# Optimization experiments

Hardware: AMD Instinct MI355X
Metric: run time of the kernel (lower is better)

The kernel has to match this reference:

```python
import jax, jax.numpy as jnp
import numpy as np

N, E, G = 8192, 65536, 16          # atoms, edges, graphs in batch
NUM_ELEM, C, NB = 10, 64, 8        # elements, hidden channels, bessel basis
LMAX, NLAYERS = 3, 2
LM = (LMAX + 1) ** 2               # 16 spherical-harmonic components
R_MAX, P_CUT = 5.0, 5
EPS = 1e-9


def spherical_harmonics(u):
    # u: [E,3] unit vectors -> real spherical harmonics l<=3, [E,16]
    x, y, z = u[:, 0], u[:, 1], u[:, 2]
    x2, y2, z2 = x * x, y * y, z * z
    sh = [
        jnp.full_like(x, 0.28209479177387814),
        0.4886025119029199 * y, 0.4886025119029199 * z, 0.4886025119029199 * x,
        1.0925484305920792 * x * y, 1.0925484305920792 * y * z,
        0.31539156525252005 * (3.0 * z2 - 1.0),
        1.0925484305920792 * x * z, 0.5462742152960396 * (x2 - y2),
        0.5900435899266435 * y * (3.0 * x2 - y2), 2.890611442640554 * x * y * z,
        0.4570457994644658 * y * (5.0 * z2 - 1.0),
        0.3731763325901154 * z * (5.0 * z2 - 3.0),
        0.4570457994644658 * x * (5.0 * z2 - 1.0),
        1.445305721320277 * z * (x2 - y2),
        0.5900435899266435 * x * (x2 - 3.0 * y2),
    ]
    return jnp.stack(sh, axis=-1)


def radial_embedding(r):
    # Bessel radial basis with polynomial envelope cutoff -> [E, NB]
    u = r / R_MAX
    p = float(P_CUT)
    cut = (1.0 - 0.5 * (p + 1.0) * (p + 2.0) * u ** P_CUT
           + p * (p + 2.0) * u ** (P_CUT + 1)
           - 0.5 * p * (p + 1.0) * u ** (P_CUT + 2))
    cut = jnp.where(u < 1.0, cut, 0.0)
    n = jnp.arange(1, NB + 1, dtype=r.dtype)
    bessel = jnp.sqrt(2.0 / R_MAX) * jnp.sin(n[None, :] * jnp.pi * u[:, None]) \
             / jnp.maximum(r, EPS)[:, None]
    return bessel * cut[:, None]


def setup_inputs() -> dict:
    key = jax.random.key(0)
    ks = jax.random.split(key, 10)
    positions = jax.random.uniform(ks[0], (N, 3), jnp.float32) * 10.0
    elems = jax.random.randint(ks[1], (N,), 0, NUM_ELEM)
    node_attrs = jax.nn.one_hot(elems, NUM_ELEM, dtype=jnp.float32)
    edge_index = jax.random.randint(ks[2], (2, E), 0, N).astype(jnp.int32)
    shifts = jnp.zeros((E, 3), jnp.float32)
    batch = jnp.sort(jax.random.randint(ks[3], (N,), 0, G)).astype(jnp.int32)
    W_embed = jax.random.normal(ks[4], (NUM_ELEM, C), jnp.float32) / np.sqrt(NUM_ELEM)
    atomic_energies_w = jnp.arange(-1.0, -(NUM_ELEM + 1.0), -1.0, dtype=jnp.float32)
    W_rad = jax.random.normal(ks[5], (NLAYERS, NB, C), jnp.float32) / np.sqrt(NB)
    W_prod = jax.random.normal(ks[6], (NLAYERS, NUM_ELEM, (LMAX + 1) * C, C),
                               jnp.float32) / np.sqrt((LMAX + 1) * C)
    w_read = jax.random.normal(ks[7], (C,), jnp.float32) / np.sqrt(C)
    return {"positions": positions, "node_attrs": node_attrs, "shifts": shifts,
            "W_embed": W_embed, "atomic_energies_w": atomic_energies_w,
            "W_rad": W_rad, "W_prod": W_prod, "w_read": w_read,
            "edge_index": edge_index, "batch": batch}


def _energy(positions, node_attrs, shifts, W_embed, atomic_energies_w,
            W_rad, W_prod, w_read, edge_index, batch):
    snd, rcv = edge_index[0], edge_index[1]
    vec = positions[rcv] - positions[snd] + shifts            # [E,3]
    length = jnp.sqrt(jnp.sum(vec * vec, axis=-1) + EPS)      # [E]
    Y = spherical_harmonics(vec / length[:, None])            # [E,LM]
    R = radial_embedding(length)                              # [E,NB]

    e0 = jax.ops.segment_sum(node_attrs @ atomic_energies_w, batch, num_segments=G)
    h = node_attrs @ W_embed                                  # [N,C]

    for layer in range(NLAYERS):
        w = R @ W_rad[layer]                                  # [E,C] radial weights
        msg = (w * h[snd])[:, None, :] * Y[:, :, None]        # [E,LM,C] tensor product
        A = jax.ops.segment_sum(msg, rcv, num_segments=N)     # [N,LM,C] atomic basis
        A2 = A * A
        # invariant (rotation-invariant) contraction: sum over m within each l
        B = jnp.concatenate(
            [A2[:, l * l:(l + 1) * (l + 1), :].sum(axis=1) for l in range(LMAX + 1)],
            axis=-1)                                          # [N,(LMAX+1)*C]
        # element-dependent product-basis mixing
        h = jnp.einsum('nf,efc,ne->nc', B, W_prod[layer], node_attrs)

    node_e = h @ w_read                                       # [N]
    inter_e = jax.ops.segment_sum(node_e, batch, num_segments=G)
    return e0 + inter_e                                       # [G]


def reference(positions, node_attrs, shifts, W_embed, atomic_energies_w,
              W_rad, W_prod, w_read, edge_index, batch):
    energy = _energy(positions, node_attrs, shifts, W_embed, atomic_energies_w,
                     W_rad, W_prod, w_read, edge_index, batch)
    forces = -jax.grad(
        lambda p: _energy(p, node_attrs, shifts, W_embed, atomic_energies_w,
                          W_rad, W_prod, w_read, edge_index, batch).sum()
    )(positions)
    return energy, forces
```

## Files before the change

### kernel.cpp

```cpp
#include <hip/hip_runtime.h>
#include <math.h>

#define NN 8192
#define NE 65536
#define NG 16
#define NEL 10
#define CC 64
#define NLM 16
#define MAXST 32
#define PI_F 3.14159265358979f

__device__ __forceinline__ int lm_l(int lm) {
    return (lm == 0) ? 0 : (lm < 4) ? 1 : (lm < 9) ? 2 : 3;
}

__device__ __forceinline__ void stage_pack(
    const float* __restrict__ PK, const int* __restrict__ SSND,
    int beg, int cnt, int c, float* sPK, int* sS)
{
    int tot = cnt * 24;
    for (int i = c; i < tot; i += 64) sPK[i] = PK[(size_t)beg*24 + i];
    if (c < cnt) sS[c] = SSND[beg + c];
    __builtin_amdgcn_wave_barrier();
}

__global__ __launch_bounds__(256) void k_front(
    const float* __restrict__ pos, const float* __restrict__ shifts,
    const int* __restrict__ snd, const int* __restrict__ rcv,
    float* __restrict__ Y, float* __restrict__ R,
    float* __restrict__ U, float* __restrict__ L, int* __restrict__ cnt,
    const float* __restrict__ attrs, const float* __restrict__ Wemb,
    const float* __restrict__ aew, const int* __restrict__ batch,
    float* __restrict__ h0, int* __restrict__ elem, int* __restrict__ ecnt,
    float* __restrict__ out,
    const float* __restrict__ Wprod1, const float* __restrict__ wread,
    float* __restrict__ vb1)
{
    __shared__ int hcnt[NEL];
    int bx = blockIdx.x;
    if (bx < 256) {
        int e = bx * 256 + threadIdx.x;
        int s = snd[e], r = rcv[e];
        float vx = pos[r*3+0] - pos[s*3+0] + shifts[e*3+0];
        float vy = pos[r*3+1] - pos[s*3+1] + shifts[e*3+1];
        float vz = pos[r*3+2] - pos[s*3+2] + shifts[e*3+2];
        float len = sqrtf(vx*vx + vy*vy + vz*vz + 1e-9f);
        L[e] = len;
        if (len >= 5.0f) return;
        atomicAdd(&cnt[r], 1);
        float x = vx/len, y = vy/len, z = vz/len;
        U[e*3+0] = x; U[e*3+1] = y; U[e*3+2] = z;
        float x2 = x*x, y2 = y*y, z2 = z*z;
        float4* Yv = (float4*)(Y + (size_t)e*16);
        Yv[0] = make_float4(0.28209479177387814f,
                            0.4886025119029199f*y,
                            0.4886025119029199f*z,
                            0.4886025119029199f*x);
        Yv[1] = make_float4(1.0925484305920792f*x*y,
                            1.0925484305920792f*y*z,
                            0.31539156525252005f*(3.f*z2 - 1.f),
                            1.0925484305920792f*x*z);
        Yv[2] = make_float4(0.5462742152960396f*(x2 - y2),
                            0.5900435899266435f*y*(3.f*x2 - y2),
                            2.890611442640554f*x*y*z,
                            0.4570457994644658f*y*(5.f*z2 - 1.f));
        Yv[3] = make_float4(0.3731763325901154f*z*(5.f*z2 - 3.f),
                            0.4570457994644658f*x*(5.f*z2 - 1.f),
                            1.445305721320277f*z*(x2 - y2),
                            0.5900435899266435f*x*(x2 - 3.f*y2));
        float ur = len * 0.2f;
        float u2 = ur*ur, u4 = u2*u2, u5 = u4*ur, u6 = u5*ur, u7 = u6*ur;
        float cut = 1.f - 21.f*u5 + 35.f*u6 - 15.f*u7;
        const float s2f = 0.632455532033676f;
        float th = (PI_F/5.f) * len;
        float s1, c1; sincosf(th, &s1, &c1);
        float sn_ = s1, cs = c1;
        float coef = s2f * cut / len;
        float rv[8];
#pragma unroll
        for (int nb = 0; nb < 8; nb++) {
            rv[nb] = coef * sn_;
            float ns = sn_*c1 + cs*s1;
            float nc = cs*c1 - sn_*s1;
            sn_ = ns; cs = nc;
        }
        float4* Rv = (float4*)(R + (size_t)e*8);
        Rv[0] = make_float4(rv[0], rv[1], rv[2], rv[3]);
        Rv[1] = make_float4(rv[4], rv[5], rv[6], rv[7]);
    } else if (bx < 768) {
        int t = threadIdx.x, c = t & 63, w = t >> 6;
        if (t < NEL) hcnt[t] = 0;
        __syncthreads();
        float esum = 0.f; int curb = -1;
        for (int g = 0; g < 4; g++) {
            int n = (bx - 256)*16 + w*4 + g;
            float hv = 0.f;
            for (int el = 0; el < NEL; el++) hv += attrs[n*NEL+el] * Wemb[el*CC+c];
            h0[(size_t)n*CC+c] = hv;
            int el = 0; float e0 = 0.f;
            for (int k = 0; k < NEL; k++) {
                float a = attrs[n*NEL+k];
                e0 += a * aew[k];
                if (a > 0.5f) el = k;
            }
            if (c == 0) {
                elem[n] = el;
                atomicAdd(&hcnt[el], 1);
            }
            int b = batch[n];
            if (b != curb) {
                if (curb >= 0 && c == 0) atomicAdd(&out[curb], esum);
                curb = b; esum = 0.f;
            }
            esum += e0;
        }
        if (curb >= 0 && c == 0) atomicAdd(&out[curb], esum);
        __syncthreads();
        if (t < NEL) { int v = hcnt[t]; if (v) atomicAdd(&ecnt[t], v); }
    } else {
        int el = bx - 768, f = threadIdx.x;
        float s = 0.f;
        for (int c = 0; c < CC; c++) s += wread[c] * Wprod1[(size_t)el*256*CC + f*CC + c];
        vb1[el*256+f] = s;
    }
}

__global__ __launch_bounds__(1024) void k_scan(
    const int* __restrict__ cnt, int* __restrict__ offs,
    const int* __restrict__ ecnt, int* __restrict__ eoff)
{
    __shared__ int wsum[16];
    int t = threadIdx.x, lane = t & 63, w = t >> 6;
    int loc[8];
    int run = 0;
#pragma unroll
    for (int i = 0; i < 8; i++) { int v = cnt[t*8+i]; loc[i] = run; run += v; }
    int v = run;
#pragma unroll
    for (int o = 1; o < 64; o <<= 1) {
        int u = __shfl_up(v, o, 64);
        if (lane >= o) v += u;
    }
    if (lane == 63) wsum[w] = v;
    __syncthreads();
    if (t < 16) {
        int x = wsum[t];
#pragma unroll
        for (int o = 1; o < 16; o <<= 1) {
            int u = __shfl_up(x, o, 64);
            if (t >= o) x += u;
        }
        wsum[t] = x;
    }
    __syncthreads();
    int wpre = (w == 0) ? 0 : wsum[w-1];
    int pre = wpre + v - run;
#pragma unroll
    for (int i = 0; i < 8; i++) offs[t*8+i] = pre + loc[i];
    if (t == 1023) offs[NN] = pre + run;
    if (t == 0) {
        int r = 0;
        for (int el = 0; el < NEL; el++) { eoff[el] = r; r += ecnt[el]; }
        eoff[NEL] = r;
    }
}

__global__ void k_scatpack(
    const int* __restrict__ snd, const int* __restrict__ rcv,
    const float* __restrict__ Y, const float* __restrict__ R,
    const float* __restrict__ U, const float* __restrict__ L,
    const int* __restrict__ offs, int* __restrict__ cur,
    float* __restrict__ PK, int* __restrict__ SSND,
    float* __restrict__ UL,
    const int* __restrict__ elem, const int* __restrict__ eoff,
    int* __restrict__ ecur, int* __restrict__ nbe)
{
    int e = blockIdx.x * blockDim.x + threadIdx.x;
    if (e < NN) {
        int el = elem[e];
        int p = eoff[el] + atomicAdd(&ecur[el], 1);
        nbe[p] = e;
    }
    if (e >= NE) return;
    if (L[e] >= 5.0f) return;
    int r = rcv[e];
    int p = offs[r] + atomicAdd(&cur[r], 1);
    const float4* Yp = (const float4*)(Y + (size_t)e*16);
    float4* d = (float4*)(PK + (size_t)p*24);
    d[0] = Yp[0]; d[1] = Yp[1]; d[2] = Yp[2]; d[3] = Yp[3];
    const float4* Rp = (const float4*)(R + (size_t)e*8);
    d[4] = Rp[0]; d[5] = Rp[1];
    SSND[p] = snd[e];
    ((float4*)UL)[p] = make_float4(U[e*3+0], U[e*3+1], U[e*3+2], L[e]);
}

__global__ __launch_bounds__(256) void k_fwd0(
    const float* __restrict__ PK, const int* __restrict__ SSND,
    const float* __restrict__ Wrad0, const float* __restrict__ Wprod0,
    const float* __restrict__ h0, const float* __restrict__ attrs,
    const int* __restrict__ elem, const int* __restrict__ offs,
    const int* __restrict__ nbe, float* __restrict__ h1,
    float* __restrict__ A0)
{
    __shared__ __align__(16) float sB[4][1024];
    __shared__ __align__(16) float sPK[4][MAXST*24];
    __shared__ int sS[4][MAXST];
    int t = threadIdx.x, c = t & 63, w = t >> 6;
    float wr[8];
#pragma unroll
    for (int nb = 0; nb < 8; nb++) wr[nb] = Wrad0[nb*CC+c];
    int nid[4], nel[4]; float na[4];
#pragma unroll
    for (int g = 0; g < 4; g++) {
        int n = nbe[blockIdx.x*16 + w*4 + g];
        nid[g] = n;
        int el = elem[n]; nel[g] = el; na[g] = attrs[n*NEL+el];
        float acc[NLM];
#pragma unroll
        for (int lm = 0; lm < NLM; lm++) acc[lm] = 0.f;
        int beg = offs[n], end = offs[n+1];
        for (int base = beg; base < end; base += MAXST) {
            int m = min(MAXST, end - base);
            stage_pack(PK, SSND, base, m, c, sPK[w], sS[w]);
            for (int cb = 0; cb < m; cb += 4) {
                float hb[4];
#pragma unroll
                for (int k = 0; k < 4; k++)
                    hb[k] = (cb+k < m) ? h0[(size_t)sS[w][cb+k]*CC + c] : 0.f;
#pragma unroll
                for (int jj = 0; jj < 4; jj++) {
                    if (cb+jj >= m) break;
                    const float* rec = &sPK[w][(cb+jj)*24];
                    float wv = 0.f;
#pragma unroll
                    for (int nb = 0; nb < 8; nb++) wv += rec[16+nb]*wr[nb];
                    float tt = wv * hb[jj];
#pragma unroll
                    for (int lm = 0; lm < NLM; lm++) acc[lm] += rec[lm]*tt;
                }
            }
            __builtin_amdgcn_wave_barrier();
        }
#pragma unroll
        for (int lm = 0; lm < NLM; lm++) A0[(size_t)n*1024 + lm*64 + c] = acc[lm];
        float b0 = acc[0]*acc[0];
        float b1 = acc[1]*acc[1] + acc[2]*acc[2] + acc[3]*acc[3];
        float b2 = acc[4]*acc[4] + acc[5]*acc[5] + acc[6]*acc[6] + acc[7]*acc[7] + acc[8]*acc[8];
        float b3 = 0.f;
#pragma unroll
        for (int lm = 9; lm < 16; lm++) b3 += acc[lm]*acc[lm];
        sB[w][g*256 + 0*64 + c] = b0;
        sB[w][g*256 + 1*64 + c] = b1;
        sB[w][g*256 + 2*64 + c] = b2;
        sB[w][g*256 + 3*64 + c] = b3;
    }
    __builtin_amdgcn_wave_barrier();
    float hv[4] = {0.f, 0.f, 0.f, 0.f};
    int done = 0;
    while (done != 0xF) {
        int g0 = __ffs(~done & 0xF) - 1;
        int el = (g0==0) ? nel[0] : (g0==1) ? nel[1] : (g0==2) ? nel[2] : nel[3];
        int msk = 0;
#pragma unroll
        for (int g = 0; g < 4; g++) if (nel[g] == el) msk |= 1 << g;
        const float* Wn = Wprod0 + (size_t)el*256*CC;
        float tmp[4] = {0.f, 0.f, 0.f, 0.f};
        for (int f4 = 0; f4 < 64; f4++) {
            float wv0 = Wn[(f4*4+0)*CC + c];
            float wv1 = Wn[(f4*4+1)*CC + c];
            float wv2 = Wn[(f4*4+2)*CC + c];
            float wv3 = Wn[(f4*4+3)*CC + c];
#pragma unroll
            for (int g = 0; g < 4; g++) {
                float4 b = *((const float4*)&sB[w][g*256 + f4*4]);
                tmp[g] += b.x*wv0 + b.y*wv1 + b.z*wv2 + b.w*wv3;
            }
        }
#pragma unroll
        for (int g = 0; g < 4; g++) if ((msk >> g) & 1) hv[g] = tmp[g];
        done |= msk;
    }
#pragma unroll
    for (int g = 0; g < 4; g++) h1[(size_t)nid[g]*CC + c] = na[g]*hv[g];
}

__global__ __launch_bounds__(256) void k_fbwd1(
    const float* __restrict__ PK, const int* __restrict__ SSND,
    const float* __restrict__ Wrad1, const float* __restrict__ h1,
    const float* __restrict__ vb1,
    const float* __restrict__ attrs, const int* __restrict__ elem,
    const int* __restrict__ batch, const int* __restrict__ offs,
    float* __restrict__ gYp, float* __restrict__ gRp, float* __restrict__ gh,
    float* __restrict__ out)
{
    __shared__ __align__(16) float wrls[8*68];
    __shared__ __align__(16) float sPK[4][MAXST*24];
    __shared__ int sS[4][MAXST];
    __shared__ __align__(16) float Mls[4][16*68];
    __shared__ __align__(16) float Tls[4][4*68];
    __shared__ __align__(16) float Gls[4][4*68];
    int t = threadIdx.x, c = t & 63, w = t >> 6;
    float wr[8];
#pragma unroll
    for (int nb = 0; nb < 8; nb++) wr[nb] = Wrad1[nb*CC+c];
    if (w == 0) {
#pragma unroll
        for (int nb = 0; nb < 8; nb++) wrls[nb*68+c] = wr[nb];
    }
    __syncthreads();
    float esum = 0.f; int curb = -1;
    for (int g = 0; g < 4; g++) {
        int n = blockIdx.x*16 + w*4 + g;
        int el = elem[n];
        float a = attrs[n*NEL+el];
        float g4[4];
#pragma unroll
        for (int l = 0; l < 4; l++) g4[l] = a * vb1[el*256 + l*64 + c];
        int beg = offs[n], end = offs[n+1];
        int cnt = end - beg;
        float acc[NLM];
#pragma unroll
        for (int lm = 0; lm < NLM; lm++) acc[lm] = 0.f;
        for (int base = beg; base < end; base += MAXST) {
            int m = min(MAXST, end - base);
            stage_pack(PK, SSND, base, m, c, sPK[w], sS[w]);
            for (int cb = 0; cb < m; cb += 4) {
                float hb[4];
#pragma unroll
                for (int k = 0; k < 4; k++)
                    hb[k] = (cb+k < m) ? h1[(size_t)sS[w][cb+k]*CC + c] : 0.f;
#pragma unroll
                for (int jj = 0; jj < 4; jj++) {
                    if (cb+jj >= m) break;
                    const float* rec = &sPK[w][(cb+jj)*24];
                    float wv = 0.f;
#pragma unroll
                    for (int nb = 0; nb < 8; nb++) wv += rec[16+nb]*wr[nb];
                    float tt = wv * hb[jj];
#pragma unroll
                    for (int lm = 0; lm < NLM; lm++) acc[lm] += rec[lm]*tt;
                }
            }
            __builtin_amdgcn_wave_barrier();
        }
        bool cached = (cnt <= MAXST);
        float b0 = acc[0]*acc[0];
        float b1 = acc[1]*acc[1] + acc[2]*acc[2] + acc[3]*acc[3];
        float b2 = acc[4]*acc[4] + acc[5]*acc[5] + acc[6]*acc[6] + acc[7]*acc[7] + acc[8]*acc[8];
        float b3 = 0.f;
#pragma unroll
        for (int lm = 9; lm < 16; lm++) b3 += acc[lm]*acc[lm];
        float ep = b0*vb1[el*256+c] + b1*vb1[el*256+64+c]
                 + b2*vb1[el*256+128+c] + b3*vb1[el*256+192+c];
#pragma unroll
        for (int o = 32; o > 0; o >>= 1) ep += __shfl_xor(ep, o, 64);
        int b = batch[n];
        if (b != curb) {
            if (curb >= 0 && c == 0) atomicAdd(&out[curb], esum);
            curb = b; esum = 0.f;
        }
        esum += a * ep;
        float M[NLM];
#pragma unroll
        for (int lm = 0; lm < NLM; lm++) {
            M[lm] = 2.f * acc[lm] * g4[lm_l(lm)];
            Mls[w][lm*68+c] = M[lm];
        }
        __builtin_amdgcn_wave_barrier();
        for (int base = beg; base < end; base += MAXST) {
            int m = min(MAXST, end - base);
            if (!cached) stage_pack(PK, SSND, base, m, c, sPK[w], sS[w]);
            for (int cb = 0; cb < m; cb += 4) {
                int ncq = min(4, m - cb);
                float hb[4];
#pragma unroll
                for (int k = 0; k < 4; k++)
                    hb[k] = (cb+k < m) ? h1[(size_t)sS[w][cb+k]*CC + c] : 0.f;
#pragma unroll
                for (int jj = 0; jj < 4; jj++) {
                    if (jj >= ncq) break;
                    const float* rec = &sPK[w][(cb+jj)*24];
                    float wv = 0.f;
#pragma unroll
                    for (int nb = 0; nb < 8; nb++) wv += rec[16+nb]*wr[nb];
                    float hvv = hb[jj];
                    float my = 0.f;
#pragma unroll
                    for (int lm = 0; lm < NLM; lm++) my += M[lm]*rec[lm];
                    Tls[w][jj*68+c] = wv * hvv;
                    Gls[w][jj*68+c] = hvv * my;
                    atomicAdd(&gh[(size_t)sS[w][cb+jj]*CC + c], wv * my);
                }
                __builtin_amdgcn_wave_barrier();
                {
                    int jj = c >> 4, lm = c & 15;
                    if (jj < ncq) {
                        const float4* mrow = (const float4*)&Mls[w][lm*68];
                        const float4* trow = (const float4*)&Tls[w][jj*68];
                        float s_ = 0.f;
#pragma unroll
                        for (int k4 = 0; k4 < 16; k4++) {
                            float4 mm = mrow[k4]; float4 tv = trow[k4];
                            s_ += mm.x*tv.x + mm.y*tv.y + mm.z*tv.z + mm.w*tv.w;
                        }
                        gYp[(size_t)(base + cb + jj)*16+lm] = s_;
                    }
                }
                if (c < 32) {
                    int jj = c >> 3, nb = c & 7;
                    if (jj < ncq) {
                        const float4* wrow = (const float4*)&wrls[nb*68];
                        const float4* grow = (const float4*)&Gls[w][jj*68];
                        float s_ = 0.f;
#pragma unroll
                        for (int k4 = 0; k4 < 16; k4++) {
                            float4 wv4 = wrow[k4]; float4 gv = grow[k4];
                            s_ += wv4.x*gv.x + wv4.y*gv.y + wv4.z*gv.z + wv4.w*gv.w;
                        }
                        gRp[(size_t)(base + cb + jj)*8+nb] = s_;
                    }
                }
                __builtin_amdgcn_wave_barrier();
            }
        }
    }
    if (curb >= 0 && c == 0) atomicAdd(&out[curb], esum);
}

__global__ __launch_bounds__(256) void k_fbwd0geo(
    const float* __restrict__ PK, const int* __restrict__ SSND,
    const float* __restrict__ Wrad0, const float* __restrict__ h0,
    const float* __restrict__ gh1, const float* __restrict__ Wprod0,
    const float* __restrict__ A0,
    const float* __restrict__ attrs, const int* __restrict__ elem,
    const int* __restrict__ offs, const int* __restrict__ nbe,
    const float* __restrict__ gYp, const float* __restrict__ gRp,
    const float* __restrict__ UL, float* __restrict__ F)
{
    __shared__ __align__(16) float wrls[8*68];
    __shared__ __align__(16) float sPK[4][MAXST*24];
    __shared__ int sS[4][MAXST];
    __shared__ __align__(16) float Mls[4][16*68];
    __shared__ __align__(16) float Tls[4][4*68];
    __shared__ __align__(16) float Gls[4][4*68];
    __shared__ __align__(16) float sgh[4][4][64];
    __shared__ float gols[4][4*24];
    int t = threadIdx.x, c = t & 63, w = t >> 6;
    float wr[8];
#pragma unroll
    for (int nb = 0; nb < 8; nb++) wr[nb] = Wrad0[nb*CC+c];
    if (w == 0) {
#pragma unroll
        for (int nb = 0; nb < 8; nb++) wrls[nb*68+c] = wr[nb];
    }
    __syncthreads();
    int nid[4], nel[4]; float na[4];
#pragma unroll
    for (int g = 0; g < 4; g++) {
        int n = nbe[blockIdx.x*16 + w*4 + g];
        nid[g] = n;
        int el = elem[n]; nel[g] = el; na[g] = attrs[n*NEL+el];
        sgh[w][g][c] = gh1[(size_t)n*CC + c];
    }
    __builtin_amdgcn_wave_barrier();
    float outv[4][4];
    int done = 0;
    while (done != 0xF) {
        int g0 = __ffs(~done & 0xF) - 1;
        int el = (g0==0) ? nel[0] : (g0==1) ? nel[1] : (g0==2) ? nel[2] : nel[3];
        int msk = 0;
#pragma unroll
        for (int g = 0; g < 4; g++) if (nel[g] == el) msk |= 1 << g;
        const float* W0 = Wprod0 + (size_t)el*256*CC;
#pragma unroll
        for (int l = 0; l < 4; l++) {
            const float4* row = (const float4*)(W0 + (size_t)(l*64 + c)*CC);
            float t4[4] = {0.f, 0.f, 0.f, 0.f};
#pragma unroll 4
            for (int k4 = 0; k4 < 16; k4++) {
                float4 wv = row[k4];
#pragma unroll
                for (int g = 0; g < 4; g++) {
                    float4 gg = *((const float4*)&sgh[w][g][k4*4]);
                    t4[g] += wv.x*gg.x + wv.y*gg.y + wv.z*gg.z + wv.w*gg.w;
                }
            }
#pragma unroll
            for (int g = 0; g < 4; g++) if ((msk >> g) & 1) outv[l][g] = t4[g];
        }
        done |= msk;
    }
    for (int g = 0; g < 4; g++) {
        int n = nid[g];
        float g4[4];
#pragma unroll
        for (int l = 0; l < 4; l++) g4[l] = na[g]*outv[l][g];
        int beg = offs[n], end = offs[n+1];
        float acc[NLM];
#pragma unroll
        for (int lm = 0; lm < NLM; lm++) acc[lm] = A0[(size_t)n*1024 + lm*64 + c];
        float M[NLM];
#pragma unroll
        for (int lm = 0; lm < NLM; lm++) {
            M[lm] = 2.f * acc[lm] * g4[lm_l(lm)];
            Mls[w][lm*68+c] = M[lm];
        }
        __builtin_amdgcn_wave_barrier();
        for (int base = beg; base < end; base += MAXST) {
            int m = min(MAXST, end - base);
            stage_pack(PK, SSND, base, m, c, sPK[w], sS[w]);
            for (int cb = 0; cb < m; cb += 4) {
                int ncq = min(4, m - cb);
                float hb[4];
#pragma unroll
                for (int k = 0; k < 4; k++)
                    hb[k] = (cb+k < m) ? h0[(size_t)sS[w][cb+k]*CC + c] : 0.f;
#pragma unroll
                for (int jj = 0; jj < 4; jj++) {
                    if (jj >= ncq) break;
                    const float* rec = &sPK[w][(cb+jj)*24];
                    float wv = 0.f;
#pragma unroll
                    for (int nb = 0; nb < 8; nb++) wv += rec[16+nb]*wr[nb];
                    float hvv = hb[jj];
                    float my = 0.f;
#pragma unroll
                    for (int lm = 0; lm < NLM; lm++) my += M[lm]*rec[lm];
                    Tls[w][jj*68+c] = wv * hvv;
                    Gls[w][jj*68+c] = hvv * my;
                }
                __builtin_amdgcn_wave_barrier();
                {
                    int jj = c >> 4, lm = c & 15;
                    if (jj < ncq) {
                        const float4* mrow = (const float4*)&Mls[w][lm*68];
                        const float4* trow = (const float4*)&Tls[w][jj*68];
                        float s_ = 0.f;
#pragma unroll
                        for (int k4 = 0; k4 < 16; k4++) {
                            float4 mm = mrow[k4]; float4 tv = trow[k4];
                            s_ += mm.x*tv.x + mm.y*tv.y + mm.z*tv.z + mm.w*tv.w;
                        }
                        gols[w][jj*24+lm] = s_ + gYp[(size_t)(base + cb + jj)*16+lm];
                    }
                }
                if (c < 32) {
                    int jj = c >> 3, nb = c & 7;
                    if (jj < ncq) {
                        const float4* wrow = (const float4*)&wrls[nb*68];
                        const float4* grow = (const float4*)&Gls[w][jj*68];
                        float s_ = 0.f;
#pragma unroll
                        for (int k4 = 0; k4 < 16; k4++) {
                            float4 wv4 = wrow[k4]; float4 gv = grow[k4];
                            s_ += wv4.x*gv.x + wv4.y*gv.y + wv4.z*gv.z + wv4.w*gv.w;
                        }
                        gols[w][jj*24+16+nb] = s_ + gRp[(size_t)(base + cb + jj)*8+nb];
                    }
                }
                __builtin_amdgcn_wave_barrier();
                if ((c & 15) == 0) {
                    int jj = c >> 4;
                    if (jj < ncq) {
                        int p = base + cb + jj;
                        const float* go = &gols[w][jj*24];
                        float4 ul = ((const float4*)UL)[p];
                        float x = ul.x, y = ul.y, z = ul.z, len = ul.w;
                        float x2 = x*x, y2 = y*y, z2 = z*z;
                        float gx = 0.f, gy = 0.f, gz = 0.f;
                        gx += 0.4886025119029199f*go[3];
                        gy += 0.4886025119029199f*go[1];
                        gz += 0.4886025119029199f*go[2];
                        gx += 1.0925484305920792f*y*go[4];  gy += 1.0925484305920792f*x*go[4];
                        gy += 1.0925484305920792f*z*go[5];  gz += 1.0925484305920792f*y*go[5];
                        gz += 1.8923493915151203f*z*go[6];
                        gx += 1.0925484305920792f*z*go[7];  gz += 1.0925484305920792f*x*go[7];
                        gx += 1.0925484305920792f*x*go[8];  gy -= 1.0925484305920792f*y*go[8];
                        gx += 3.540261539559861f*x*y*go[9];
                        gy += 0.5900435899266435f*(3.f*x2 - 3.f*y2)*go[9];
                        gx += 2.890611442640554f*y*z*go[10]; gy += 2.890611442640554f*x*z*go[10]; gz += 2.890611442640554f*x*y*go[10];
                        gy += 0.4570457994644658f*(5.f*z2 - 1.f)*go[11]; gz += 4.570457994644658f*y*z*go[11];
                        gz += 0.3731763325901154f*(15.f*z2 - 3.f)*go[12];
                        gx += 0.4570457994644658f*(5.f*z2 - 1.f)*go[13]; gz += 4.570457994644658f*x*z*go[13];
                        gx += 2.890611442640554f*x*z*go[14]; gy -= 2.890611442640554f*y*z*go[14];
                        gz += 1.445305721320277f*(x2 - y2)*go[14];
                        gx += 0.5900435899266435f*(3.f*x2 - 3.f*y2)*go[15];
                        gy -= 3.540261539559861f*x*y*go[15];
                        float ur = len * 0.2f;
                        float u2 = ur*ur, u4 = u2*u2, u5 = u4*ur, u6 = u5*ur, u7 = u6*ur;
                        float poly  = 1.f - 21.f*u5 + 35.f*u6 - 15.f*u7;
                        float dpoly = (-105.f*u4 + 210.f*u5 - 105.f*u6)*0.2f;
                        const float s2f = 0.632455532033676f;
                        const float k1 = PI_F/5.f;
                        float th = k1*len;
                        float s1, c1; sincosf(th, &s1, &c1);
                        float sn_ = s1, cs = c1;
                        float inv_r = 1.f/len;
                        bool tiny = (len < 2e-3f);
                        float gL = 0.f;
#pragma unroll
                        for (int nb = 0; nb < 8; nb++) {
                            float kn = k1*(float)(nb+1);
                            float bes = s2f*sn_*inv_r;
                            float dbes;
                            if (tiny) dbes = -s2f*kn*kn*kn*len*(1.f/3.f);
                            else      dbes = s2f*(kn*cs - sn_*inv_r)*inv_r;
                            gL += go[16+nb]*(dbes*poly + bes*dpoly);
                            float ns = sn_*c1 + cs*s1;
                            float nc = cs*c1 - sn_*s1;
                            sn_ = ns; cs = nc;
                        }
                        float dot = gx*x + gy*y + gz*z;
                        float gvx = (gx - dot*x)*inv_r + gL*x;
                        float gvy = (gy - dot*y)*inv_r + gL*y;
                        float gvz = (gz - dot*z)*inv_r + gL*z;
                        int sn2 = sS[w][cb+jj];
                        atomicAdd(&F[n*3+0], -gvx);
                        atomicAdd(&F[n*3+1], -gvy);
                        atomicAdd(&F[n*3+2], -gvz);
                        atomicAdd(&F[sn2*3+0],  gvx);
                        atomicAdd(&F[sn2*3+1],  gvy);
                        atomicAdd(&F[sn2*3+2],  gvz);
                    }
                }
                __builtin_amdgcn_wave_barrier();
            }
        }
    }
}

extern "C" void kernel_launch(void* const* d_in, const int* in_sizes, int n_in,
                              void* d_out, int out_size, void* d_ws, size_t ws_size,
                              hipStream_t stream)
{
    const float* positions  = (const float*)d_in[0];
    const float* node_attrs = (const float*)d_in[1];
    const float* shifts     = (const float*)d_in[2];
    const float* W_embed    = (const float*)d_in[3];
    const float* aew        = (const float*)d_in[4];
    const float* W_rad      = (const float*)d_in[5];
    const float* W_prod     = (const float*)d_in[6];
    const float* w_read     = (const float*)d_in[7];
    const int*   edge_index = (const int*)d_in[8];
    const int*   batch      = (const int*)d_in[9];
    float* out = (float*)d_out;

    const int* snd = edge_index;
    const int* rcv = edge_index + NE;

    char* ws = (char*)d_ws;
    size_t off = 0;
    auto allocf = [&](size_t nelems) -> float* {
        float* p = (float*)(ws + off); off += nelems * sizeof(float); return p;
    };
    float* Y    = allocf((size_t)NE*16);
    float* R    = allocf((size_t)NE*8);
    float* U    = allocf((size_t)NE*3);
    float* L    = allocf((size_t)NE);
    float* PK   = allocf((size_t)NE*24);
    float* UL   = allocf((size_t)NE*4);
    float* H0   = allocf((size_t)NN*CC);
    float* H1   = allocf((size_t)NN*CC);
    float* A0   = allocf((size_t)NN*1024);
    float* GYP  = allocf((size_t)NE*16);
    float* GRP  = allocf((size_t)NE*8);
    float* VB1  = allocf((size_t)NEL*256);
    size_t zero_off = off;
    float* GH1  = allocf((size_t)NN*CC);
    int* CNT   = (int*)(ws + off); off += (size_t)NN*4;
    int* CUR   = (int*)(ws + off); off += (size_t)NN*4;
    int* ECNT  = (int*)(ws + off); off += 16*4;
    int* ECUR  = (int*)(ws + off); off += 16*4;
    size_t zero_bytes = off - zero_off;
    int* ELEM  = (int*)(ws + off); off += (size_t)NN*4;
    int* OFFS  = (int*)(ws + off); off += (size_t)(NN+1)*4;
    int* SSND  = (int*)(ws + off); off += (size_t)NE*4;
    int* ELOFF = (int*)(ws + off); off += 16*4;
    int* NBE   = (int*)(ws + off); off += (size_t)NN*4;

    hipMemsetAsync(out, 0, (size_t)out_size * sizeof(float), stream);
    hipMemsetAsync(ws + zero_off, 0, zero_bytes, stream);

    const float* Wrad0  = W_rad;
    const float* Wrad1  = W_rad + 8*CC;
    const float* Wprod0 = W_prod;
    const float* Wprod1 = W_prod + (size_t)NEL*256*CC;

    k_front<<<256 + 512 + NEL, 256, 0, stream>>>(
        positions, shifts, snd, rcv, Y, R, U, L, CNT,
        node_attrs, W_embed, aew, batch, H0, ELEM, ECNT, out,
        Wprod1, w_read, VB1);
    k_scan<<<1, 1024, 0, stream>>>(CNT, OFFS, ECNT, ELOFF);
    k_scatpack<<<NE/256, 256, 0, stream>>>(snd, rcv, Y, R, U, L, OFFS, CUR,
                                           PK, SSND, UL, ELEM, ELOFF, ECUR, NBE);

    k_fwd0<<<NN/16, 256, 0, stream>>>(PK, SSND, Wrad0, Wprod0, H0, node_attrs, ELEM,
                                      OFFS, NBE, H1, A0);
    k_fbwd1<<<NN/16, 256, 0, stream>>>(PK, SSND, Wrad1, H1, VB1, node_attrs, ELEM,
                                       batch, OFFS, GYP, GRP, GH1, out);
    k_fbwd0geo<<<NN/16, 256, 0, stream>>>(PK, SSND, Wrad0, H0, GH1, Wprod0, A0,
                                          node_attrs, ELEM, OFFS, NBE,
                                          GYP, GRP, UL, out + NG);
    (void)in_sizes; (void)n_in; (void)ws_size;
}
```

Measured before the change: 275.1 us.

## Fuse all pipeline stages into one cooperative persistent kernel with grid syncs

Replaces the sequence of memsets and six kernel launches with a single cooperative kernel of 256 blocks. It runs each stage, including front, scan, scatter-pack and the three layer passes, as a loop over work groups separated by grid-wide barriers. The stage bodies become device functions sharing one shared-memory struct. The goal is to remove launch overhead and inter-kernel gaps, at the cost of grid-sync latency, fewer resident blocks (256) for the node-parallel stages, and a larger shared-memory footprint per block. A fallback path keeps the multi-kernel launches if cooperative launch fails.

Result: slower. 689.2 us (+150.5%).

```diff
diff --git a/kernel.cpp b/kernel.cpp
--- a/kernel.cpp
+++ b/kernel.cpp
@@ -1,5 +1,8 @@
 #include <hip/hip_runtime.h>
+#include <hip/hip_cooperative_groups.h>
 #include <math.h>
+
+namespace cg = cooperative_groups;
 
 #define NN 8192
 #define NE 65536
@@ -9,228 +12,77 @@
 #define NLM 16
 #define MAXST 32
 #define PI_F 3.14159265358979f
+#define GRIDB 256
+#define GSZ (GRIDB*256)
 
 __device__ __forceinline__ int lm_l(int lm) {
     return (lm == 0) ? 0 : (lm < 4) ? 1 : (lm < 9) ? 2 : 3;
 }
 
-__device__ __forceinline__ void stage_pack(
-    const float* __restrict__ PK, const int* __restrict__ SSND,
-    int beg, int cnt, int c, float* sPK, int* sS)
-{
-    int tot = cnt * 24;
-    for (int i = c; i < tot; i += 64) sPK[i] = PK[(size_t)beg*24 + i];
-    if (c < cnt) sS[c] = SSND[beg + c];
+struct Prm {
+    const float *pos, *shifts;
+    const int *snd, *rcv;
+    float *Y, *R, *U, *L;
+    int *cnt, *cur;
+    const float *attrs, *Wemb, *aew;
+    const int *batch;
+    float *h0, *h1;
+    int *elem, *ecnt, *ecur, *eoff, *nbe, *offs;
+    float *out;
+    const float *Wrad0, *Wrad1, *Wprod0, *Wprod1, *wread;
+    float *vb1;
+    float *PK; int *SSND; float *UL;
+    float *A0, *gYp, *gRp, *gh1;
+};
+
+struct Shm {
+    float wrls[8*68];
+    int   sS[4][MAXST];
+    float sPK[4][MAXST*24];
+    float Mls[4][1088];
+    float Tls[4][4*68];
+    float Gls[4][4*68];
+    float sgh[4][4][64];
+    float gols[4][96];
+};
+
+__device__ __forceinline__ void stage(const Prm& p, int base, int m, int c,
+                                      float* sPKw, int* sSw)
+{
+    int tot = m * 24;
+    for (int i = c; i < tot; i += 64) sPKw[i] = p.PK[(size_t)base*24 + i];
+    if (c < m) sSw[c] = p.SSND[base + c];
     __builtin_amdgcn_wave_barrier();
 }
 
-__global__ __launch_bounds__(256) void k_front(
-    const float* __restrict__ pos, const float* __restrict__ shifts,
-    const int* __restrict__ snd, const int* __restrict__ rcv,
-    float* __restrict__ Y, float* __restrict__ R,
-    float* __restrict__ U, float* __restrict__ L, int* __restrict__ cnt,
-    const float* __restrict__ attrs, const float* __restrict__ Wemb,
-    const float* __restrict__ aew, const int* __restrict__ batch,
-    float* __restrict__ h0, int* __restrict__ elem, int* __restrict__ ecnt,
-    float* __restrict__ out,
-    const float* __restrict__ Wprod1, const float* __restrict__ wread,
-    float* __restrict__ vb1)
-{
-    __shared__ int hcnt[NEL];
-    int bx = blockIdx.x;
-    if (bx < 256) {
-        int e = bx * 256 + threadIdx.x;
-        int s = snd[e], r = rcv[e];
-        float vx = pos[r*3+0] - pos[s*3+0] + shifts[e*3+0];
-        float vy = pos[r*3+1] - pos[s*3+1] + shifts[e*3+1];
-        float vz = pos[r*3+2] - pos[s*3+2] + shifts[e*3+2];
-        float len = sqrtf(vx*vx + vy*vy + vz*vz + 1e-9f);
-        L[e] = len;
-        if (len >= 5.0f) return;
-        atomicAdd(&cnt[r], 1);
-        float x = vx/len, y = vy/len, z = vz/len;
-        U[e*3+0] = x; U[e*3+1] = y; U[e*3+2] = z;
-        float x2 = x*x, y2 = y*y, z2 = z*z;
-        float4* Yv = (float4*)(Y + (size_t)e*16);
-        Yv[0] = make_float4(0.28209479177387814f,
-                            0.4886025119029199f*y,
-                            0.4886025119029199f*z,
-                            0.4886025119029199f*x);
-        Yv[1] = make_float4(1.0925484305920792f*x*y,
-                            1.0925484305920792f*y*z,
-                            0.31539156525252005f*(3.f*z2 - 1.f),
-                            1.0925484305920792f*x*z);
-        Yv[2] = make_float4(0.5462742152960396f*(x2 - y2),
-                            0.5900435899266435f*y*(3.f*x2 - y2),
-                            2.890611442640554f*x*y*z,
-                            0.4570457994644658f*y*(5.f*z2 - 1.f));
-        Yv[3] = make_float4(0.3731763325901154f*z*(5.f*z2 - 3.f),
-                            0.4570457994644658f*x*(5.f*z2 - 1.f),
-                            1.445305721320277f*z*(x2 - y2),
-                            0.5900435899266435f*x*(x2 - 3.f*y2));
-        float ur = len * 0.2f;
-        float u2 = ur*ur, u4 = u2*u2, u5 = u4*ur, u6 = u5*ur, u7 = u6*ur;
-        float cut = 1.f - 21.f*u5 + 35.f*u6 - 15.f*u7;
-        const float s2f = 0.632455532033676f;
-        float th = (PI_F/5.f) * len;
-        float s1, c1; sincosf(th, &s1, &c1);
-        float sn_ = s1, cs = c1;
-        float coef = s2f * cut / len;
-        float rv[8];
-#pragma unroll
-        for (int nb = 0; nb < 8; nb++) {
-            rv[nb] = coef * sn_;
-            float ns = sn_*c1 + cs*s1;
-            float nc = cs*c1 - sn_*s1;
-            sn_ = ns; cs = nc;
-        }
-        float4* Rv = (float4*)(R + (size_t)e*8);
-        Rv[0] = make_float4(rv[0], rv[1], rv[2], rv[3]);
-        Rv[1] = make_float4(rv[4], rv[5], rv[6], rv[7]);
-    } else if (bx < 768) {
-        int t = threadIdx.x, c = t & 63, w = t >> 6;
-        if (t < NEL) hcnt[t] = 0;
-        __syncthreads();
-        float esum = 0.f; int curb = -1;
-        for (int g = 0; g < 4; g++) {
-            int n = (bx - 256)*16 + w*4 + g;
-            float hv = 0.f;
-            for (int el = 0; el < NEL; el++) hv += attrs[n*NEL+el] * Wemb[el*CC+c];
-            h0[(size_t)n*CC+c] = hv;
-            int el = 0; float e0 = 0.f;
-            for (int k = 0; k < NEL; k++) {
-                float a = attrs[n*NEL+k];
-                e0 += a * aew[k];
-                if (a > 0.5f) el = k;
-            }
-            if (c == 0) {
-                elem[n] = el;
-                atomicAdd(&hcnt[el], 1);
-            }
-            int b = batch[n];
-            if (b != curb) {
-                if (curb >= 0 && c == 0) atomicAdd(&out[curb], esum);
-                curb = b; esum = 0.f;
-            }
-            esum += e0;
-        }
-        if (curb >= 0 && c == 0) atomicAdd(&out[curb], esum);
-        __syncthreads();
-        if (t < NEL) { int v = hcnt[t]; if (v) atomicAdd(&ecnt[t], v); }
-    } else {
-        int el = bx - 768, f = threadIdx.x;
-        float s = 0.f;
-        for (int c = 0; c < CC; c++) s += wread[c] * Wprod1[(size_t)el*256*CC + f*CC + c];
-        vb1[el*256+f] = s;
-    }
-}
-
-__global__ __launch_bounds__(1024) void k_scan(
-    const int* __restrict__ cnt, int* __restrict__ offs,
-    const int* __restrict__ ecnt, int* __restrict__ eoff)
-{
-    __shared__ int wsum[16];
-    int t = threadIdx.x, lane = t & 63, w = t >> 6;
-    int loc[8];
-    int run = 0;
-#pragma unroll
-    for (int i = 0; i < 8; i++) { int v = cnt[t*8+i]; loc[i] = run; run += v; }
-    int v = run;
-#pragma unroll
-    for (int o = 1; o < 64; o <<= 1) {
-        int u = __shfl_up(v, o, 64);
-        if (lane >= o) v += u;
-    }
-    if (lane == 63) wsum[w] = v;
-    __syncthreads();
-    if (t < 16) {
-        int x = wsum[t];
-#pragma unroll
-        for (int o = 1; o < 16; o <<= 1) {
-            int u = __shfl_up(x, o, 64);
-            if (t >= o) x += u;
-        }
-        wsum[t] = x;
-    }
-    __syncthreads();
-    int wpre = (w == 0) ? 0 : wsum[w-1];
-    int pre = wpre + v - run;
-#pragma unroll
-    for (int i = 0; i < 8; i++) offs[t*8+i] = pre + loc[i];
-    if (t == 1023) offs[NN] = pre + run;
-    if (t == 0) {
-        int r = 0;
-        for (int el = 0; el < NEL; el++) { eoff[el] = r; r += ecnt[el]; }
-        eoff[NEL] = r;
-    }
-}
-
-__global__ void k_scatpack(
-    const int* __restrict__ snd, const int* __restrict__ rcv,
-    const float* __restrict__ Y, const float* __restrict__ R,
-    const float* __restrict__ U, const float* __restrict__ L,
-    const int* __restrict__ offs, int* __restrict__ cur,
-    float* __restrict__ PK, int* __restrict__ SSND,
-    float* __restrict__ UL,
-    const int* __restrict__ elem, const int* __restrict__ eoff,
-    int* __restrict__ ecur, int* __restrict__ nbe)
-{
-    int e = blockIdx.x * blockDim.x + threadIdx.x;
-    if (e < NN) {
-        int el = elem[e];
-        int p = eoff[el] + atomicAdd(&ecur[el], 1);
-        nbe[p] = e;
-    }
-    if (e >= NE) return;
-    if (L[e] >= 5.0f) return;
-    int r = rcv[e];
-    int p = offs[r] + atomicAdd(&cur[r], 1);
-    const float4* Yp = (const float4*)(Y + (size_t)e*16);
-    float4* d = (float4*)(PK + (size_t)p*24);
-    d[0] = Yp[0]; d[1] = Yp[1]; d[2] = Yp[2]; d[3] = Yp[3];
-    const float4* Rp = (const float4*)(R + (size_t)e*8);
-    d[4] = Rp[0]; d[5] = Rp[1];
-    SSND[p] = snd[e];
-    ((float4*)UL)[p] = make_float4(U[e*3+0], U[e*3+1], U[e*3+2], L[e]);
-}
-
-__global__ __launch_bounds__(256) void k_fwd0(
-    const float* __restrict__ PK, const int* __restrict__ SSND,
-    const float* __restrict__ Wrad0, const float* __restrict__ Wprod0,
-    const float* __restrict__ h0, const float* __restrict__ attrs,
-    const int* __restrict__ elem, const int* __restrict__ offs,
-    const int* __restrict__ nbe, float* __restrict__ h1,
-    float* __restrict__ A0)
-{
-    __shared__ __align__(16) float sB[4][1024];
-    __shared__ __align__(16) float sPK[4][MAXST*24];
-    __shared__ int sS[4][MAXST];
-    int t = threadIdx.x, c = t & 63, w = t >> 6;
+__device__ void dev_fwd0(const Prm& p, int grp, int t, Shm& sh)
+{
+    int c = t & 63, w = t >> 6;
     float wr[8];
 #pragma unroll
-    for (int nb = 0; nb < 8; nb++) wr[nb] = Wrad0[nb*CC+c];
+    for (int nb = 0; nb < 8; nb++) wr[nb] = p.Wrad0[nb*CC+c];
     int nid[4], nel[4]; float na[4];
 #pragma unroll
     for (int g = 0; g < 4; g++) {
-        int n = nbe[blockIdx.x*16 + w*4 + g];
+        int n = p.nbe[grp*16 + w*4 + g];
         nid[g] = n;
-        int el = elem[n]; nel[g] = el; na[g] = attrs[n*NEL+el];
+        int el = p.elem[n]; nel[g] = el; na[g] = p.attrs[n*NEL+el];
         float acc[NLM];
 #pragma unroll
         for (int lm = 0; lm < NLM; lm++) acc[lm] = 0.f;
-        int beg = offs[n], end = offs[n+1];
+        int beg = p.offs[n], end = p.offs[n+1];
         for (int base = beg; base < end; base += MAXST) {
             int m = min(MAXST, end - base);
-            stage_pack(PK, SSND, base, m, c, sPK[w], sS[w]);
+            stage(p, base, m, c, sh.sPK[w], sh.sS[w]);
             for (int cb = 0; cb < m; cb += 4) {
                 float hb[4];
 #pragma unroll
                 for (int k = 0; k < 4; k++)
-                    hb[k] = (cb+k < m) ? h0[(size_t)sS[w][cb+k]*CC + c] : 0.f;
+                    hb[k] = (cb+k < m) ? p.h0[(size_t)sh.sS[w][cb+k]*CC + c] : 0.f;
 #pragma unroll
                 for (int jj = 0; jj < 4; jj++) {
                     if (cb+jj >= m) break;
-                    const float* rec = &sPK[w][(cb+jj)*24];
+                    const float* rec = &sh.sPK[w][(cb+jj)*24];
                     float wv = 0.f;
 #pragma unroll
                     for (int nb = 0; nb < 8; nb++) wv += rec[16+nb]*wr[nb];
@@ -242,17 +94,17 @@
             __builtin_amdgcn_wave_barrier();
         }
 #pragma unroll
-        for (int lm = 0; lm < NLM; lm++) A0[(size_t)n*1024 + lm*64 + c] = acc[lm];
+        for (int lm = 0; lm < NLM; lm++) p.A0[(size_t)nid[g]*1024 + lm*64 + c] = acc[lm];
         float b0 = acc[0]*acc[0];
         float b1 = acc[1]*acc[1] + acc[2]*acc[2] + acc[3]*acc[3];
         float b2 = acc[4]*acc[4] + acc[5]*acc[5] + acc[6]*acc[6] + acc[7]*acc[7] + acc[8]*acc[8];
         float b3 = 0.f;
 #pragma unroll
         for (int lm = 9; lm < 16; lm++) b3 += acc[lm]*acc[lm];
-        sB[w][g*256 + 0*64 + c] = b0;
-        sB[w][g*256 + 1*64 + c] = b1;
-        sB[w][g*256 + 2*64 + c] = b2;
-        sB[w][g*256 + 3*64 + c] = b3;
+        sh.Mls[w][g*256 + 0*64 + c] = b0;
+        sh.Mls[w][g*256 + 1*64 + c] = b1;
+        sh.Mls[w][g*256 + 2*64 + c] = b2;
+        sh.Mls[w][g*256 + 3*64 + c] = b3;
     }
     __builtin_amdgcn_wave_barrier();
     float hv[4] = {0.f, 0.f, 0.f, 0.f};
@@ -263,7 +115,7 @@
         int msk = 0;
 #pragma unroll
         for (int g = 0; g < 4; g++) if (nel[g] == el) msk |= 1 << g;
-        const float* Wn = Wprod0 + (size_t)el*256*CC;
+        const float* Wn = p.Wprod0 + (size_t)el*256*CC;
         float tmp[4] = {0.f, 0.f, 0.f, 0.f};
         for (int f4 = 0; f4 < 64; f4++) {
             float wv0 = Wn[(f4*4+0)*CC + c];
@@ -272,7 +124,7 @@
             float wv3 = Wn[(f4*4+3)*CC + c];
 #pragma unroll
             for (int g = 0; g < 4; g++) {
-                float4 b = *((const float4*)&sB[w][g*256 + f4*4]);
+                float4 b = *((const float4*)&sh.Mls[w][g*256 + f4*4]);
                 tmp[g] += b.x*wv0 + b.y*wv1 + b.z*wv2 + b.w*wv3;
             }
         }
@@ -281,58 +133,45 @@
         done |= msk;
     }
 #pragma unroll
-    for (int g = 0; g < 4; g++) h1[(size_t)nid[g]*CC + c] = na[g]*hv[g];
-}
-
-__global__ __launch_bounds__(256) void k_fbwd1(
-    const float* __restrict__ PK, const int* __restrict__ SSND,
-    const float* __restrict__ Wrad1, const float* __restrict__ h1,
-    const float* __restrict__ vb1,
-    const float* __restrict__ attrs, const int* __restrict__ elem,
-    const int* __restrict__ batch, const int* __restrict__ offs,
-    float* __restrict__ gYp, float* __restrict__ gRp, float* __restrict__ gh,
-    float* __restrict__ out)
-{
-    __shared__ __align__(16) float wrls[8*68];
-    __shared__ __align__(16) float sPK[4][MAXST*24];
-    __shared__ int sS[4][MAXST];
-    __shared__ __align__(16) float Mls[4][16*68];
-    __shared__ __align__(16) float Tls[4][4*68];
-    __shared__ __align__(16) float Gls[4][4*68];
-    int t = threadIdx.x, c = t & 63, w = t >> 6;
+    for (int g = 0; g < 4; g++) p.h1[(size_t)nid[g]*CC + c] = na[g]*hv[g];
+}
+
+__device__ void dev_fbwd1(const Prm& p, int grp, int t, Shm& sh)
+{
+    int c = t & 63, w = t >> 6;
     float wr[8];
 #pragma unroll
-    for (int nb = 0; nb < 8; nb++) wr[nb] = Wrad1[nb*CC+c];
+    for (int nb = 0; nb < 8; nb++) wr[nb] = p.Wrad1[nb*CC+c];
     if (w == 0) {
 #pragma unroll
-        for (int nb = 0; nb < 8; nb++) wrls[nb*68+c] = wr[nb];
+        for (int nb = 0; nb < 8; nb++) sh.wrls[nb*68+c] = wr[nb];
     }
     __syncthreads();
     float esum = 0.f; int curb = -1;
     for (int g = 0; g < 4; g++) {
-        int n = blockIdx.x*16 + w*4 + g;
-        int el = elem[n];
-        float a = attrs[n*NEL+el];
+        int n = grp*16 + w*4 + g;
+        int el = p.elem[n];
+        float a = p.attrs[n*NEL+el];
         float g4[4];
 #pragma unroll
-        for (int l = 0; l < 4; l++) g4[l] = a * vb1[el*256 + l*64 + c];
-        int beg = offs[n], end = offs[n+1];
-        int cnt = end - beg;
+        for (int l = 0; l < 4; l++) g4[l] = a * p.vb1[el*256 + l*64 + c];
+        int beg = p.offs[n], end = p.offs[n+1];
+        int cnt2 = end - beg;
         float acc[NLM];
 #pragma unroll
         for (int lm = 0; lm < NLM; lm++) acc[lm] = 0.f;
         for (int base = beg; base < end; base += MAXST) {
             int m = min(MAXST, end - base);
-            stage_pack(PK, SSND, base, m, c, sPK[w], sS[w]);
+            stage(p, base, m, c, sh.sPK[w], sh.sS[w]);
             for (int cb = 0; cb < m; cb += 4) {
                 float hb[4];
 #pragma unroll
                 for (int k = 0; k < 4; k++)
-                    hb[k] = (cb+k < m) ? h1[(size_t)sS[w][cb+k]*CC + c] : 0.f;
+                    hb[k] = (cb+k < m) ? p.h1[(size_t)sh.sS[w][cb+k]*CC + c] : 0.f;
 #pragma unroll
                 for (int jj = 0; jj < 4; jj++) {
                     if (cb+jj >= m) break;
-                    const float* rec = &sPK[w][(cb+jj)*24];
+                    const float* rec = &sh.sPK[w][(cb+jj)*24];
                     float wv = 0.f;
 #pragma unroll
                     for (int nb = 0; nb < 8; nb++) wv += rec[16+nb]*wr[nb];
@@ -343,20 +182,20 @@
             }
             __builtin_amdgcn_wave_barrier();
         }
-        bool cached = (cnt <= MAXST);
+        bool cached = (cnt2 <= MAXST);
         float b0 = acc[0]*acc[0];
         float b1 = acc[1]*acc[1] + acc[2]*acc[2] + acc[3]*acc[3];
         float b2 = acc[4]*acc[4] + acc[5]*acc[5] + acc[6]*acc[6] + acc[7]*acc[7] + acc[8]*acc[8];
         float b3 = 0.f;
 #pragma unroll
         for (int lm = 9; lm < 16; lm++) b3 += acc[lm]*acc[lm];
-        float ep = b0*vb1[el*256+c] + b1*vb1[el*256+64+c]
-                 + b2*vb1[el*256+128+c] + b3*vb1[el*256+192+c];
+        float ep = b0*p.vb1[el*256+c] + b1*p.vb1[el*256+64+c]
+                 + b2*p.vb1[el*256+128+c] + b3*p.vb1[el*256+192+c];
 #pragma unroll
         for (int o = 32; o > 0; o >>= 1) ep += __shfl_xor(ep, o, 64);
-        int b = batch[n];
+        int b = p.batch[n];
         if (b != curb) {
-            if (curb >= 0 && c == 0) atomicAdd(&out[curb], esum);
+            if (curb >= 0 && c == 0) atomicAdd(&p.out[curb], esum);
             curb = b; esum = 0.f;
         }
         esum += a * ep;
@@ -364,22 +203,22 @@
 #pragma unroll
         for (int lm = 0; lm < NLM; lm++) {
             M[lm] = 2.f * acc[lm] * g4[lm_l(lm)];
-            Mls[w][lm*68+c] = M[lm];
+            sh.Mls[w][lm*68+c] = M[lm];
         }
         __builtin_amdgcn_wave_barrier();
         for (int base = beg; base < end; base += MAXST) {
             int m = min(MAXST, end - base);
-            if (!cached) stage_pack(PK, SSND, base, m, c, sPK[w], sS[w]);
+            if (!cached) stage(p, base, m, c, sh.sPK[w], sh.sS[w]);
             for (int cb = 0; cb < m; cb += 4) {
                 int ncq = min(4, m - cb);
                 float hb[4];
 #pragma unroll
                 for (int k = 0; k < 4; k++)
-                    hb[k] = (cb+k < m) ? h1[(size_t)sS[w][cb+k]*CC + c] : 0.f;
+                    hb[k] = (cb+k < m) ? p.h1[(size_t)sh.sS[w][cb+k]*CC + c] : 0.f;
 #pragma unroll
                 for (int jj = 0; jj < 4; jj++) {
                     if (jj >= ncq) break;
-                    const float* rec = &sPK[w][(cb+jj)*24];
+                    const float* rec = &sh.sPK[w][(cb+jj)*24];
                     float wv = 0.f;
 #pragma unroll
                     for (int nb = 0; nb < 8; nb++) wv += rec[16+nb]*wr[nb];
@@ -387,80 +226,65 @@
                     float my = 0.f;
 #pragma unroll
                     for (int lm = 0; lm < NLM; lm++) my += M[lm]*rec[lm];
-                    Tls[w][jj*68+c] = wv * hvv;
-                    Gls[w][jj*68+c] = hvv * my;
-                    atomicAdd(&gh[(size_t)sS[w][cb+jj]*CC + c], wv * my);
+                    sh.Tls[w][jj*68+c] = wv * hvv;
+                    sh.Gls[w][jj*68+c] = hvv * my;
+                    atomicAdd(&p.gh1[(size_t)sh.sS[w][cb+jj]*CC + c], wv * my);
                 }
                 __builtin_amdgcn_wave_barrier();
                 {
                     int jj = c >> 4, lm = c & 15;
                     if (jj < ncq) {
-                        const float4* mrow = (const float4*)&Mls[w][lm*68];
-                        const float4* trow = (const float4*)&Tls[w][jj*68];
+                        const float4* mrow = (const float4*)&sh.Mls[w][lm*68];
+                        const float4* trow = (const float4*)&sh.Tls[w][jj*68];
                         float s_ = 0.f;
 #pragma unroll
                         for (int k4 = 0; k4 < 16; k4++) {
                             float4 mm = mrow[k4]; float4 tv = trow[k4];
                             s_ += mm.x*tv.x + mm.y*tv.y + mm.z*tv.z + mm.w*tv.w;
                         }
-                        gYp[(size_t)(base + cb + jj)*16+lm] = s_;
+                        p.gYp[(size_t)(base + cb + jj)*16+lm] = s_;
                     }
                 }
                 if (c < 32) {
                     int jj = c >> 3, nb = c & 7;
                     if (jj < ncq) {
-                        const float4* wrow = (const float4*)&wrls[nb*68];
-                        const float4* grow = (const float4*)&Gls[w][jj*68];
+                        const float4* wrow = (const float4*)&sh.wrls[nb*68];
+                        const float4* grow = (const float4*)&sh.Gls[w][jj*68];
                         float s_ = 0.f;
 #pragma unroll
                         for (int k4 = 0; k4 < 16; k4++) {
                             float4 wv4 = wrow[k4]; float4 gv = grow[k4];
                             s_ += wv4.x*gv.x + wv4.y*gv.y + wv4.z*gv.z + wv4.w*gv.w;
                         }
-                        gRp[(size_t)(base + cb + jj)*8+nb] = s_;
+                        p.gRp[(size_t)(base + cb + jj)*8+nb] = s_;
                     }
                 }
                 __builtin_amdgcn_wave_barrier();
             }
         }
     }
-    if (curb >= 0 && c == 0) atomicAdd(&out[curb], esum);
-}
-
-__global__ __launch_bounds__(256) void k_fbwd0geo(
-    const float* __restrict__ PK, const int* __restrict__ SSND,
-    const float* __restrict__ Wrad0, const float* __restrict__ h0,
-    const float* __restrict__ gh1, const float* __restrict__ Wprod0,
-    const float* __restrict__ A0,
-    const float* __restrict__ attrs, const int* __restrict__ elem,
-    const int* __restrict__ offs, const int* __restrict__ nbe,
-    const float* __restrict__ gYp, const float* __restrict__ gRp,
-    const float* __restrict__ UL, float* __restrict__ F)
-{
-    __shared__ __align__(16) float wrls[8*68];
-    __shared__ __align__(16) float sPK[4][MAXST*24];
-    __shared__ int sS[4][MAXST];
-    __shared__ __align__(16) float Mls[4][16*68];
-    __shared__ __align__(16) float Tls[4][4*68];
-    __shared__ __align__(16) float Gls[4][4*68];
-    __shared__ __align__(16) float sgh[4][4][64];
-    __shared__ float gols[4][4*24];
-    int t = threadIdx.x, c = t & 63, w = t >> 6;
+    if (curb >= 0 && c == 0) atomicAdd(&p.out[curb], esum);
+}
+
+__device__ void dev_fbwd0geo(const Prm& p, int grp, int t, Shm& sh)
+{
+    int c = t & 63, w = t >> 6;
+    float* F = p.out + NG;
     float wr[8];
 #pragma unroll
-    for (int nb = 0; nb < 8; nb++) wr[nb] = Wrad0[nb*CC+c];
+    for (int nb = 0; nb < 8; nb++) wr[nb] = p.Wrad0[nb*CC+c];
     if (w == 0) {
 #pragma unroll
-        for (int nb = 0; nb < 8; nb++) wrls[nb*68+c] = wr[nb];
+        for (int nb = 0; nb < 8; nb++) sh.wrls[nb*68+c] = wr[nb];
     }
     __syncthreads();
     int nid[4], nel[4]; float na[4];
 #pragma unroll
     for (int g = 0; g < 4; g++) {
-        int n = nbe[blockIdx.x*16 + w*4 + g];
+        int n = p.nbe[grp*16 + w*4 + g];
         nid[g] = n;
-        int el = elem[n]; nel[g] = el; na[g] = attrs[n*NEL+el];
-        sgh[w][g][c] = gh1[(size_t)n*CC + c];
+        int el = p.elem[n]; nel[g] = el; na[g] = p.attrs[n*NEL+el];
+        sh.sgh[w][g][c] = p.gh1[(size_t)n*CC + c];
     }
     __builtin_amdgcn_wave_barrier();
     float outv[4][4];
@@ -471,7 +295,7 @@
         int msk = 0;
 #pragma unroll
         for (int g = 0; g < 4; g++) if (nel[g] == el) msk |= 1 << g;
-        const float* W0 = Wprod0 + (size_t)el*256*CC;
+        const float* W0 = p.Wprod0 + (size_t)el*256*CC;
 #pragma unroll
         for (int l = 0; l < 4; l++) {
             const float4* row = (const float4*)(W0 + (size_t)(l*64 + c)*CC);
@@ -481,7 +305,7 @@
                 float4 wv = row[k4];
 #pragma unroll
                 for (int g = 0; g < 4; g++) {
-                    float4 gg = *((const float4*)&sgh[w][g][k4*4]);
+                    float4 gg = *((const float4*)&sh.sgh[w][g][k4*4]);
                     t4[g] += wv.x*gg.x + wv.y*gg.y + wv.z*gg.z + wv.w*gg.w;
                 }
             }
@@ -495,30 +319,30 @@
         float g4[4];
 #pragma unroll
         for (int l = 0; l < 4; l++) g4[l] = na[g]*outv[l][g];
-        int beg = offs[n], end = offs[n+1];
+        int beg = p.offs[n], end = p.offs[n+1];
         float acc[NLM];
 #pragma unroll
-        for (int lm = 0; lm < NLM; lm++) acc[lm] = A0[(size_t)n*1024 + lm*64 + c];
+        for (int lm = 0; lm < NLM; lm++) acc[lm] = p.A0[(size_t)n*1024 + lm*64 + c];
         float M[NLM];
 #pragma unroll
         for (int lm = 0; lm < NLM; lm++) {
             M[lm] = 2.f * acc[lm] * g4[lm_l(lm)];
-            Mls[w][lm*68+c] = M[lm];
+            sh.Mls[w][lm*68+c] = M[lm];
         }
         __builtin_amdgcn_wave_barrier();
         for (int base = beg; base < end; base += MAXST) {
             int m = min(MAXST, end - base);
-            stage_pack(PK, SSND, base, m, c, sPK[w], sS[w]);
+            stage(p, base, m, c, sh.sPK[w], sh.sS[w]);
             for (int cb = 0; cb < m; cb += 4) {
                 int ncq = min(4, m - cb);
                 float hb[4];
 #pragma unroll
                 for (int k = 0; k < 4; k++)
-                    hb[k] = (cb+k < m) ? h0[(size_t)sS[w][cb+k]*CC + c] : 0.f;
+                    hb[k] = (cb+k < m) ? p.h0[(size_t)sh.sS[w][cb+k]*CC + c] : 0.f;
 #pragma unroll
                 for (int jj = 0; jj < 4; jj++) {
                     if (jj >= ncq) break;
-                    const float* rec = &sPK[w][(cb+jj)*24];
+                    const float* rec = &sh.sPK[w][(cb+jj)*24];
                     float wv = 0.f;
 #pragma unroll
                     for (int nb = 0; nb < 8; nb++) wv += rec[16+nb]*wr[nb];
@@ -526,45 +350,45 @@
                     float my = 0.f;
 #pragma unroll
                     for (int lm = 0; lm < NLM; lm++) my += M[lm]*rec[lm];
-                    Tls[w][jj*68+c] = wv * hvv;
-                    Gls[w][jj*68+c] = hvv * my;
+                    sh.Tls[w][jj*68+c] = wv * hvv;
+                    sh.Gls[w][jj*68+c] = hvv * my;
                 }
                 __builtin_amdgcn_wave_barrier();
                 {
                     int jj = c >> 4, lm = c & 15;
                     if (jj < ncq) {
-                        const float4* mrow = (const float4*)&Mls[w][lm*68];
-                        const float4* trow = (const float4*)&Tls[w][jj*68];
+                        const float4* mrow = (const float4*)&sh.Mls[w][lm*68];
+                        const float4* trow = (const float4*)&sh.Tls[w][jj*68];
                         float s_ = 0.f;
 #pragma unroll
                         for (int k4 = 0; k4 < 16; k4++) {
                             float4 mm = mrow[k4]; float4 tv = trow[k4];
                             s_ += mm.x*tv.x + mm.y*tv.y + mm.z*tv.z + mm.w*tv.w;
                         }
-                        gols[w][jj*24+lm] = s_ + gYp[(size_t)(base + cb + jj)*16+lm];
+                        sh.gols[w][jj*24+lm] = s_ + p.gYp[(size_t)(base + cb + jj)*16+lm];
                     }
                 }
                 if (c < 32) {
                     int jj = c >> 3, nb = c & 7;
                     if (jj < ncq) {
-                        const float4* wrow = (const float4*)&wrls[nb*68];
-                        const float4* grow = (const float4*)&Gls[w][jj*68];
+                        const float4* wrow = (const float4*)&sh.wrls[nb*68];
+                        const float4* grow = (const float4*)&sh.Gls[w][jj*68];
                         float s_ = 0.f;
 #pragma unroll
                         for (int k4 = 0; k4 < 16; k4++) {
                             float4 wv4 = wrow[k4]; float4 gv = grow[k4];
                             s_ += wv4.x*gv.x + wv4.y*gv.y + wv4.z*gv.z + wv4.w*gv.w;
                         }
-                        gols[w][jj*24+16+nb] = s_ + gRp[(size_t)(base + cb + jj)*8+nb];
+                        sh.gols[w][jj*24+16+nb] = s_ + p.gRp[(size_t)(base + cb + jj)*8+nb];
                     }
                 }
                 __builtin_amdgcn_wave_barrier();
                 if ((c & 15) == 0) {
                     int jj = c >> 4;
                     if (jj < ncq) {
-                        int p = base + cb + jj;
-                        const float* go = &gols[w][jj*24];
-                        float4 ul = ((const float4*)UL)[p];
+                        int pp = base + cb + jj;
+                        const float* go = &sh.gols[w][jj*24];
+                        float4 ul = ((const float4*)p.UL)[pp];
                         float x = ul.x, y = ul.y, z = ul.z, len = ul.w;
                         float x2 = x*x, y2 = y*y, z2 = z*z;
                         float gx = 0.f, gy = 0.f, gz = 0.f;
@@ -614,7 +438,7 @@
                         float gvx = (gx - dot*x)*inv_r + gL*x;
                         float gvy = (gy - dot*y)*inv_r + gL*y;
                         float gvz = (gz - dot*z)*inv_r + gL*z;
-                        int sn2 = sS[w][cb+jj];
+                        int sn2 = sh.sS[w][cb+jj];
                         atomicAdd(&F[n*3+0], -gvx);
                         atomicAdd(&F[n*3+1], -gvy);
                         atomicAdd(&F[n*3+2], -gvz);
@@ -629,77 +453,339 @@
     }
 }
 
+__device__ void dev_geom_edge(const Prm& p, int e)
+{
+    int s = p.snd[e], r = p.rcv[e];
+    float vx = p.pos[r*3+0] - p.pos[s*3+0] + p.shifts[e*3+0];
+    float vy = p.pos[r*3+1] - p.pos[s*3+1] + p.shifts[e*3+1];
+    float vz = p.pos[r*3+2] - p.pos[s*3+2] + p.shifts[e*3+2];
+    float len = sqrtf(vx*vx + vy*vy + vz*vz + 1e-9f);
+    p.L[e] = len;
+    if (len >= 5.0f) return;
+    atomicAdd(&p.cnt[r], 1);
+    float x = vx/len, y = vy/len, z = vz/len;
+    p.U[e*3+0] = x; p.U[e*3+1] = y; p.U[e*3+2] = z;
+    float x2 = x*x, y2 = y*y, z2 = z*z;
+    float4* Yv = (float4*)(p.Y + (size_t)e*16);
+    Yv[0] = make_float4(0.28209479177387814f,
+                        0.4886025119029199f*y,
+                        0.4886025119029199f*z,
+                        0.4886025119029199f*x);
+    Yv[1] = make_float4(1.0925484305920792f*x*y,
+                        1.0925484305920792f*y*z,
+                        0.31539156525252005f*(3.f*z2 - 1.f),
+                        1.0925484305920792f*x*z);
+    Yv[2] = make_float4(0.5462742152960396f*(x2 - y2),
+                        0.5900435899266435f*y*(3.f*x2 - y2),
+                        2.890611442640554f*x*y*z,
+                        0.4570457994644658f*y*(5.f*z2 - 1.f));
+    Yv[3] = make_float4(0.3731763325901154f*z*(5.f*z2 - 3.f),
+                        0.4570457994644658f*x*(5.f*z2 - 1.f),
+                        1.445305721320277f*z*(x2 - y2),
+                        0.5900435899266435f*x*(x2 - 3.f*y2));
+    float ur = len * 0.2f;
+    float u2 = ur*ur, u4 = u2*u2, u5 = u4*ur, u6 = u5*ur, u7 = u6*ur;
+    float cut = 1.f - 21.f*u5 + 35.f*u6 - 15.f*u7;
+    const float s2f = 0.632455532033676f;
+    float th = (PI_F/5.f) * len;
+    float s1, c1; sincosf(th, &s1, &c1);
+    float sn_ = s1, cs = c1;
+    float coef = s2f * cut / len;
+    float rv[8];
+#pragma unroll
+    for (int nb = 0; nb < 8; nb++) {
+        rv[nb] = coef * sn_;
+        float ns = sn_*c1 + cs*s1;
+        float nc = cs*c1 - sn_*s1;
+        sn_ = ns; cs = nc;
+    }
+    float4* Rv = (float4*)(p.R + (size_t)e*8);
+    Rv[0] = make_float4(rv[0], rv[1], rv[2], rv[3]);
+    Rv[1] = make_float4(rv[4], rv[5], rv[6], rv[7]);
+}
+
+__device__ void dev_pack_edge(const Prm& p, int e)
+{
+    if (p.L[e] >= 5.0f) return;
+    int r = p.rcv[e];
+    int pp = p.offs[r] + atomicAdd(&p.cur[r], 1);
+    const float4* Yp = (const float4*)(p.Y + (size_t)e*16);
+    float4* d = (float4*)(p.PK + (size_t)pp*24);
+    d[0] = Yp[0]; d[1] = Yp[1]; d[2] = Yp[2]; d[3] = Yp[3];
+    const float4* Rp = (const float4*)(p.R + (size_t)e*8);
+    d[4] = Rp[0]; d[5] = Rp[1];
+    p.SSND[pp] = p.snd[e];
+    ((float4*)p.UL)[pp] = make_float4(p.U[e*3+0], p.U[e*3+1], p.U[e*3+2], p.L[e]);
+}
+
+__global__ __launch_bounds__(256) void k_mega(Prm p)
+{
+    cg::grid_group grid = cg::this_grid();
+    __shared__ Shm sh;
+    __shared__ int swsum[4];
+    int t = threadIdx.x, c = t & 63, w = t >> 6;
+    int bid = blockIdx.x;
+    int gtid = bid*256 + t;
+
+    for (int i = gtid; i < NN*CC; i += GSZ) p.gh1[i] = 0.f;
+    for (int i = gtid; i < NN; i += GSZ) { p.cnt[i] = 0; p.cur[i] = 0; }
+    if (gtid < 16) { p.ecnt[gtid] = 0; p.ecur[gtid] = 0; }
+    for (int i = gtid; i < NG + NN*3; i += GSZ) p.out[i] = 0.f;
+    __threadfence();
+    grid.sync();
+
+    if (gtid < NE) dev_geom_edge(p, gtid);
+    for (int idx = gtid; idx < NN*CC; idx += GSZ) {
+        int n = idx >> 6, cc = idx & 63;
+        float hv = 0.f;
+        for (int el = 0; el < NEL; el++) hv += p.attrs[n*NEL+el] * p.Wemb[el*CC+cc];
+        p.h0[idx] = hv;
+    }
+    if (gtid < NN) {
+        int n = gtid;
+        int el = 0; float e0 = 0.f;
+        for (int k = 0; k < NEL; k++) {
+            float a = p.attrs[n*NEL+k];
+            e0 += a * p.aew[k];
+            if (a > 0.5f) el = k;
+        }
+        p.elem[n] = el;
+        atomicAdd(&p.ecnt[el], 1);
+        atomicAdd(&p.out[p.batch[n]], e0);
+    }
+    if (gtid < NEL*256) {
+        int el = gtid >> 8, f = gtid & 255;
+        float s = 0.f;
+        for (int cc = 0; cc < CC; cc++) s += p.wread[cc] * p.Wprod1[(size_t)el*256*CC + f*CC + cc];
+        p.vb1[el*256+f] = s;
+    }
+    __threadfence();
+    grid.sync();
+
+    if (bid == 0) {
+        int run = 0;
+        for (int i = 0; i < 32; i++) run += p.cnt[t*32+i];
+        int v = run;
+#pragma unroll
+        for (int o = 1; o < 64; o <<= 1) {
+            int u = __shfl_up(v, o, 64);
+            if (c >= o) v += u;
+        }
+        if (c == 63) swsum[w] = v;
+        __syncthreads();
+        if (t < 4) {
+            int x = swsum[t];
+#pragma unroll
+            for (int o = 1; o < 4; o <<= 1) {
+                int u = __shfl_up(x, o, 64);
+                if (t >= o) x += u;
+            }
+            swsum[t] = x;
+        }
+        __syncthreads();
+        int wpre = (w == 0) ? 0 : swsum[w-1];
+        int acc = wpre + v - run;
+        for (int i = 0; i < 32; i++) {
+            int cv = p.cnt[t*32+i];
+            p.offs[t*32+i] = acc;
+            acc += cv;
+        }
+        if (t == 255) p.offs[NN] = acc;
+        if (t == 0) {
+            int r = 0;
+            for (int el = 0; el < NEL; el++) { p.eoff[el] = r; r += p.ecnt[el]; }
+            p.eoff[NEL] = r;
+        }
+    }
+    __threadfence();
+    grid.sync();
+
+    if (gtid < NN) {
+        int el = p.elem[gtid];
+        int pos2 = p.eoff[el] + atomicAdd(&p.ecur[el], 1);
+        p.nbe[pos2] = gtid;
+    }
+    if (gtid < NE) dev_pack_edge(p, gtid);
+    __threadfence();
+    grid.sync();
+
+    for (int rep = 0; rep < 2; rep++) dev_fwd0(p, bid + rep*GRIDB, t, sh);
+    __threadfence();
+    grid.sync();
+
+    for (int rep = 0; rep < 2; rep++) dev_fbwd1(p, bid + rep*GRIDB, t, sh);
+    __threadfence();
+    grid.sync();
+
+    for (int rep = 0; rep < 2; rep++) dev_fbwd0geo(p, bid + rep*GRIDB, t, sh);
+}
+
+__global__ __launch_bounds__(256) void k_front(Prm p)
+{
+    __shared__ int hcnt[NEL];
+    int bx = blockIdx.x;
+    if (bx < 256) {
+        dev_geom_edge(p, bx*256 + threadIdx.x);
+    } else if (bx < 768) {
+        int t = threadIdx.x, c = t & 63, w = t >> 6;
+        if (t < NEL) hcnt[t] = 0;
+        __syncthreads();
+        float esum = 0.f; int curb = -1;
+        for (int g = 0; g < 4; g++) {
+            int n = (bx - 256)*16 + w*4 + g;
+            float hv = 0.f;
+            for (int el = 0; el < NEL; el++) hv += p.attrs[n*NEL+el] * p.Wemb[el*CC+c];
+            p.h0[(size_t)n*CC+c] = hv;
+            int el = 0; float e0 = 0.f;
+            for (int k = 0; k < NEL; k++) {
+                float a = p.attrs[n*NEL+k];
+                e0 += a * p.aew[k];
+                if (a > 0.5f) el = k;
+            }
+            if (c == 0) { p.elem[n] = el; atomicAdd(&hcnt[el], 1); }
+            int b = p.batch[n];
+            if (b != curb) {
+                if (curb >= 0 && c == 0) atomicAdd(&p.out[curb], esum);
+                curb = b; esum = 0.f;
+            }
+            esum += e0;
+        }
+        if (curb >= 0 && c == 0) atomicAdd(&p.out[curb], esum);
+        __syncthreads();
+        if (threadIdx.x < NEL) { int v = hcnt[threadIdx.x]; if (v) atomicAdd(&p.ecnt[threadIdx.x], v); }
+    } else {
+        int el = bx - 768, f = threadIdx.x;
+        float s = 0.f;
+        for (int cc = 0; cc < CC; cc++) s += p.wread[cc] * p.Wprod1[(size_t)el*256*CC + f*CC + cc];
+        p.vb1[el*256+f] = s;
+    }
+}
+
+__global__ __launch_bounds__(1024) void k_scanK(Prm p)
+{
+    __shared__ int wsum[16];
+    int t = threadIdx.x, lane = t & 63, w = t >> 6;
+    int loc[8];
+    int run = 0;
+#pragma unroll
+    for (int i = 0; i < 8; i++) { int v = p.cnt[t*8+i]; loc[i] = run; run += v; }
+    int v = run;
+#pragma unroll
+    for (int o = 1; o < 64; o <<= 1) {
+        int u = __shfl_up(v, o, 64);
+        if (lane >= o) v += u;
+    }
+    if (lane == 63) wsum[w] = v;
+    __syncthreads();
+    if (t < 16) {
+        int x = wsum[t];
+#pragma unroll
+        for (int o = 1; o < 16; o <<= 1) {
+            int u = __shfl_up(x, o, 64);
+            if (t >= o) x += u;
+        }
+        wsum[t] = x;
+    }
+    __syncthreads();
+    int wpre = (w == 0) ? 0 : wsum[w-1];
+    int pre = wpre + v - run;
+#pragma unroll
+    for (int i = 0; i < 8; i++) p.offs[t*8+i] = pre + loc[i];
+    if (t == 1023) p.offs[NN] = pre + run;
+    if (t == 0) {
+        int r = 0;
+        for (int el = 0; el < NEL; el++) { p.eoff[el] = r; r += p.ecnt[el]; }
+        p.eoff[NEL] = r;
+    }
+}
+
+__global__ void k_scatpackK(Prm p)
+{
+    int e = blockIdx.x * blockDim.x + threadIdx.x;
+    if (e < NN) {
+        int el = p.elem[e];
+        int pp = p.eoff[el] + atomicAdd(&p.ecur[el], 1);
+        p.nbe[pp] = e;
+    }
+    if (e >= NE) return;
+    dev_pack_edge(p, e);
+}
+
+__global__ __launch_bounds__(256) void k_fwd0K(Prm p)
+{ __shared__ Shm sh; dev_fwd0(p, blockIdx.x, threadIdx.x, sh); }
+
+__global__ __launch_bounds__(256) void k_fbwd1K(Prm p)
+{ __shared__ Shm sh; dev_fbwd1(p, blockIdx.x, threadIdx.x, sh); }
+
+__global__ __launch_bounds__(256) void k_fbwd0geoK(Prm p)
+{ __shared__ Shm sh; dev_fbwd0geo(p, blockIdx.x, threadIdx.x, sh); }
+
 extern "C" void kernel_launch(void* const* d_in, const int* in_sizes, int n_in,
                               void* d_out, int out_size, void* d_ws, size_t ws_size,
                               hipStream_t stream)
 {
-    const float* positions  = (const float*)d_in[0];
-    const float* node_attrs = (const float*)d_in[1];
-    const float* shifts     = (const float*)d_in[2];
-    const float* W_embed    = (const float*)d_in[3];
-    const float* aew        = (const float*)d_in[4];
-    const float* W_rad      = (const float*)d_in[5];
-    const float* W_prod     = (const float*)d_in[6];
-    const float* w_read     = (const float*)d_in[7];
-    const int*   edge_index = (const int*)d_in[8];
-    const int*   batch      = (const int*)d_in[9];
-    float* out = (float*)d_out;
-
-    const int* snd = edge_index;
-    const int* rcv = edge_index + NE;
+    Prm p;
+    p.pos    = (const float*)d_in[0];
+    p.attrs  = (const float*)d_in[1];
+    p.shifts = (const float*)d_in[2];
+    p.Wemb   = (const float*)d_in[3];
+    p.aew    = (const float*)d_in[4];
+    const float* W_rad  = (const float*)d_in[5];
+    const float* W_prod = (const float*)d_in[6];
+    p.wread  = (const float*)d_in[7];
+    const int* edge_index = (const int*)d_in[8];
+    p.batch  = (const int*)d_in[9];
+    p.out = (float*)d_out;
+    p.snd = edge_index;
+    p.rcv = edge_index + NE;
+    p.Wrad0  = W_rad;
+    p.Wrad1  = W_rad + 8*CC;
+    p.Wprod0 = W_prod;
+    p.Wprod1 = W_prod + (size_t)NEL*256*CC;
 
     char* ws = (char*)d_ws;
     size_t off = 0;
     auto allocf = [&](size_t nelems) -> float* {
-        float* p = (float*)(ws + off); off += nelems * sizeof(float); return p;
+        float* q = (float*)(ws + off); off += nelems * sizeof(float); return q;
     };
-    float* Y    = allocf((size_t)NE*16);
-    float* R    = allocf((size_t)NE*8);
-    float* U    = allocf((size_t)NE*3);
-    float* L    = allocf((size_t)NE);
-    float* PK   = allocf((size_t)NE*24);
-    float* UL   = allocf((size_t)NE*4);
-    float* H0   = allocf((size_t)NN*CC);
-    float* H1   = allocf((size_t)NN*CC);
-    float* A0   = allocf((size_t)NN*1024);
-    float* GYP  = allocf((size_t)NE*16);
-    float* GRP  = allocf((size_t)NE*8);
-    float* VB1  = allocf((size_t)NEL*256);
+    p.Y    = allocf((size_t)NE*16);
+    p.R    = allocf((size_t)NE*8);
+    p.U    = allocf((size_t)NE*3);
+    p.L    = allocf((size_t)NE);
+    p.PK   = allocf((size_t)NE*24);
+    p.UL   = allocf((size_t)NE*4);
+    p.h0   = allocf((size_t)NN*CC);
+    p.h1   = allocf((size_t)NN*CC);
+    p.A0   = allocf((size_t)NN*1024);
+    p.gYp  = allocf((size_t)NE*16);
+    p.gRp  = allocf((size_t)NE*8);
+    p.vb1  = allocf((size_t)NEL*256);
     size_t zero_off = off;
-    float* GH1  = allocf((size_t)NN*CC);
-    int* CNT   = (int*)(ws + off); off += (size_t)NN*4;
-    int* CUR   = (int*)(ws + off); off += (size_t)NN*4;
-    int* ECNT  = (int*)(ws + off); off += 16*4;
-    int* ECUR  = (int*)(ws + off); off += 16*4;
+    p.gh1  = allocf((size_t)NN*CC);
+    p.cnt  = (int*)(ws + off); off += (size_t)NN*4;
+    p.cur  = (int*)(ws + off); off += (size_t)NN*4;
+    p.ecnt = (int*)(ws + off); off += 16*4;
+    p.ecur = (int*)(ws + off); off += 16*4;
     size_t zero_bytes = off - zero_off;
-    int* ELEM  = (int*)(ws + off); off += (size_t)NN*4;
-    int* OFFS  = (int*)(ws + off); off += (size_t)(NN+1)*4;
-    int* SSND  = (int*)(ws + off); off += (size_t)NE*4;
-    int* ELOFF = (int*)(ws + off); off += 16*4;
-    int* NBE   = (int*)(ws + off); off += (size_t)NN*4;
-
-    hipMemsetAsync(out, 0, (size_t)out_size * sizeof(float), stream);
-    hipMemsetAsync(ws + zero_off, 0, zero_bytes, stream);
-
-    const float* Wrad0  = W_rad;
-    const float* Wrad1  = W_rad + 8*CC;
-    const float* Wprod0 = W_prod;
-    const float* Wprod1 = W_prod + (size_t)NEL*256*CC;
-
-    k_front<<<256 + 512 + NEL, 256, 0, stream>>>(
-        positions, shifts, snd, rcv, Y, R, U, L, CNT,
-        node_attrs, W_embed, aew, batch, H0, ELEM, ECNT, out,
-        Wprod1, w_read, VB1);
-    k_scan<<<1, 1024, 0, stream>>>(CNT, OFFS, ECNT, ELOFF);
-    k_scatpack<<<NE/256, 256, 0, stream>>>(snd, rcv, Y, R, U, L, OFFS, CUR,
-                                           PK, SSND, UL, ELEM, ELOFF, ECUR, NBE);
-
-    k_fwd0<<<NN/16, 256, 0, stream>>>(PK, SSND, Wrad0, Wprod0, H0, node_attrs, ELEM,
-                                      OFFS, NBE, H1, A0);
-    k_fbwd1<<<NN/16, 256, 0, stream>>>(PK, SSND, Wrad1, H1, VB1, node_attrs, ELEM,
-                                       batch, OFFS, GYP, GRP, GH1, out);
-    k_fbwd0geo<<<NN/16, 256, 0, stream>>>(PK, SSND, Wrad0, H0, GH1, Wprod0, A0,
-                                          node_attrs, ELEM, OFFS, NBE,
-                                          GYP, GRP, UL, out + NG);
+    p.elem = (int*)(ws + off); off += (size_t)NN*4;
+    p.offs = (int*)(ws + off); off += (size_t)(NN+1)*4;
+    p.SSND = (int*)(ws + off); off += (size_t)NE*4;
+    p.eoff = (int*)(ws + off); off += 16*4;
+    p.nbe  = (int*)(ws + off); off += (size_t)NN*4;
+
+    void* args[] = { &p };
+    hipError_t err = hipLaunchCooperativeKernel((const void*)k_mega,
+                                                dim3(GRIDB), dim3(256), args, 0, stream);
+    if (err != hipSuccess) {
+        (void)hipGetLastError();
+        hipMemsetAsync(p.out, 0, (size_t)out_size * sizeof(float), stream);
+        hipMemsetAsync(ws + zero_off, 0, zero_bytes, stream);
+        k_front<<<256 + 512 + NEL, 256, 0, stream>>>(p);
+        k_scanK<<<1, 1024, 0, stream>>>(p);
+        k_scatpackK<<<NE/256, 256, 0, stream>>>(p);
+        k_fwd0K<<<NN/16, 256, 0, stream>>>(p);
+        k_fbwd1K<<<NN/16, 256, 0, stream>>>(p);
+        k_fbwd0geoK<<<NN/16, 256, 0, stream>>>(p);
+    }
     (void)in_sizes; (void)n_in; (void)ws_size;
 }
```
